# Kernel optimization log

Hardware: AMD Instinct MI355X
Metric: run time of the kernel (lower is better)

## Reference

```python
import jax, jax.numpy as jnp
import numpy as np

STRIDES = (4, 8, 16, 32, 64, 128)
MAPS = (128, 64, 32, 16, 8, 4)
VAR0, VAR1 = 0.1, 0.2
CLS_TH, NMS_TH, FINAL_TH = 0.05, 0.3, 0.5


def _decode_scale(ocls, oreg, stride):
    # ocls: [1,2,H,W], oreg: [1,4,H,W] -> dets [H*W, 5] = (x1,y1,x2,y2,score)
    prob = jax.nn.softmax(ocls, axis=1)[0, 1]          # [H,W] face probability
    H, W = prob.shape
    s = jnp.float32(stride)
    pcx = s / 2 + jnp.arange(W, dtype=jnp.float32)[None, :] * s   # prior center x
    pcy = s / 2 + jnp.arange(H, dtype=jnp.float32)[:, None] * s   # prior center y
    pwh = s * 4.0                                                 # prior w = h = 4*stride
    loc = oreg[0]                                                 # [4,H,W]
    cx = pcx + loc[0] * VAR0 * pwh
    cy = pcy + loc[1] * VAR0 * pwh
    w = pwh * jnp.exp(loc[2] * VAR1)
    h = pwh * jnp.exp(loc[3] * VAR1)
    x1 = cx - w / 2
    y1 = cy - h / 2
    x2 = x1 + w
    y2 = y1 + h
    return jnp.stack([x1.ravel(), y1.ravel(), x2.ravel(), y2.ravel(), prob.ravel()], axis=1)


def _nms_keep(dets, valid):
    # Greedy NMS (torch-style, +1 box convention), fixed trip count, returns keep mask.
    N = dets.shape[0]
    scores = jnp.where(valid, dets[:, 4], -jnp.inf)
    order = jnp.argsort(-scores)            # descending by score, invalid last
    b = dets[order]
    v = valid[order]
    x1, y1, x2, y2 = b[:, 0], b[:, 1], b[:, 2], b[:, 3]
    areas = (x2 - x1 + 1.0) * (y2 - y1 + 1.0)
    pos = jnp.arange(N)

    def body(i, carry):
        sup, keep = carry
        active = jnp.logical_and(jnp.logical_not(sup[i]), v[i])
        keep = keep.at[i].set(active)
        xx1 = jnp.maximum(x1[i], x1)
        yy1 = jnp.maximum(y1[i], y1)
        xx2 = jnp.minimum(x2[i], x2)
        yy2 = jnp.minimum(y2[i], y2)
        w = jnp.maximum(xx2 - xx1 + 1.0, 0.0)
        h = jnp.maximum(yy2 - yy1 + 1.0, 0.0)
        inter = w * h
        iou = inter / (areas[i] + areas - inter)
        sup = sup | (active & (iou > NMS_TH) & (pos > i))
        return sup, keep

    sup0 = jnp.logical_not(v)
    _, keep_sorted = jax.lax.fori_loop(0, N, body, (sup0, jnp.zeros(N, dtype=bool)))
    return jnp.zeros(N, dtype=bool).at[order].set(keep_sorted)


def _forward(ol1, ol2, ol3, ol4, ol5, ol6, ol7, ol8, ol9, ol10, ol11, ol12):
    olist = [ol1, ol2, ol3, ol4, ol5, ol6, ol7, ol8, ol9, ol10, ol11, ol12]
    dets = jnp.concatenate(
        [_decode_scale(olist[2 * i], olist[2 * i + 1], STRIDES[i]) for i in range(6)],
        axis=0)                              # [N,5]
    valid = dets[:, 4] > CLS_TH              # threshold stage (score > 0.05)
    # NMS selection is index logic -> constant w.r.t. differentiation
    keep = _nms_keep(jax.lax.stop_gradient(dets), valid)
    final = keep & (dets[:, 4] > FINAL_TH)   # post-NMS score > 0.5 filter
    # fixed-shape equivalent of gathering kept rows: zero out non-kept rows
    return dets * final[:, None].astype(dets.dtype)


def setup_inputs() -> dict:
    key = jax.random.key(0)
    inp = {}
    for i, hw in enumerate(MAPS):
        kc, kr, key = jax.random.split(key, 3)
        inp[f"ol{2 * i + 1}"] = jax.random.normal(kc, (1, 2, hw, hw), dtype=jnp.float32)
        inp[f"ol{2 * i + 2}"] = jax.random.normal(kr, (1, 4, hw, hw), dtype=jnp.float32)
    return inp


def reference(ol1, ol2, ol3, ol4, ol5, ol6, ol7, ol8, ol9, ol10, ol11, ol12):
    return _forward(ol1, ol2, ol3, ol4, ol5, ol6, ol7, ol8, ol9, ol10, ol11, ol12)
```

## Files before the change

kernel.cpp:

```cpp
#include <hip/hip_runtime.h>
#include <stdint.h>

#define N_TOTAL 21840
#define NA      21888
#define W_MAX   342
#define TOT_ENT 3753792u
#define NMS_TH  0.3f
#define FINAL_TH 0.5f
#define NSLICE  8
#define SLOTS   11
#define SCAN_T  768
#define NPUSH   11
#define GRP     4
#define NBAND   7
#define GMAX    86

struct Inputs { const float* cls[6]; const float* reg[6]; };

__device__ __forceinline__ void block_bar() {
  asm volatile("s_waitcnt lgkmcnt(0)\n\ts_barrier" ::: "memory");
}

__device__ __forceinline__ unsigned rowbase_u(unsigned r) {
  unsigned w = r >> 6, l = r & 63u;
  return 64u * (342u * w - (w * (w - 1u)) / 2u) + l * (342u - w);
}

__global__ void decode_kernel(Inputs in,
                              float* __restrict__ dx1, float* __restrict__ dy1,
                              float* __restrict__ dx2, float* __restrict__ dy2,
                              float* __restrict__ dsc,
                              unsigned long long* __restrict__ ckey,
                              unsigned int* __restrict__ Mc,
                              unsigned int* __restrict__ rank32,
                              unsigned int* __restrict__ cnt,
                              float* __restrict__ out) {
#pragma clang fp contract(off)
  int gid = blockIdx.x * blockDim.x + threadIdx.x;
  if (gid >= N_TOTAL) return;

  rank32[gid] = 0u;
  cnt[gid] = 0u;
  if (gid < NA - N_TOTAL) cnt[N_TOTAL + gid] = 0u;

  int sc, local;
  if      (gid < 16384) { sc = 0; local = gid;         }
  else if (gid < 20480) { sc = 1; local = gid - 16384; }
  else if (gid < 21504) { sc = 2; local = gid - 20480; }
  else if (gid < 21760) { sc = 3; local = gid - 21504; }
  else if (gid < 21824) { sc = 4; local = gid - 21760; }
  else                  { sc = 5; local = gid - 21824; }

  const int Wd     = 128 >> sc;
  const int stride = 4 << sc;
  const int HW     = Wd * Wd;
  const int x = local & (Wd - 1);
  const int y = local >> (7 - sc);

  const float* cls = in.cls[sc];
  const float* reg = in.reg[sc];

  float c0 = cls[local];
  float c1 = cls[HW + local];
  float m  = fmaxf(c0, c1);
  float e0 = expf(c0 - m);
  float e1 = expf(c1 - m);
  float prob = e1 / (e0 + e1);

  float l0 = reg[local];
  float l1 = reg[HW + local];
  float l2 = reg[2 * HW + local];
  float l3 = reg[3 * HW + local];

  float sF  = (float)stride;
  float pcx = 0.5f * sF + (float)x * sF;
  float pcy = 0.5f * sF + (float)y * sF;
  float pwh = sF * 4.0f;

  float cx = pcx + ((l0 * 0.1f) * pwh);
  float cy = pcy + ((l1 * 0.1f) * pwh);
  float w  = pwh * expf(l2 * 0.2f);
  float h  = pwh * expf(l3 * 0.2f);
  float x1 = cx - w * 0.5f;
  float y1 = cy - h * 0.5f;
  float x2 = x1 + w;
  float y2 = y1 + h;

  dx1[gid] = x1; dy1[gid] = y1; dx2[gid] = x2; dy2[gid] = y2; dsc[gid] = prob;

  out[gid * 5 + 0] = 0.0f;
  out[gid * 5 + 1] = 0.0f;
  out[gid * 5 + 2] = 0.0f;
  out[gid * 5 + 3] = 0.0f;
  out[gid * 5 + 4] = 0.0f;

  if (prob > FINAL_TH) {
    unsigned int pos = atomicAdd(Mc, 1u);
    ckey[pos] = ((unsigned long long)__float_as_uint(prob) << 32) |
                (unsigned int)(~(unsigned int)gid);
  }
}

__global__ void __launch_bounds__(256)
rank_kernel(const unsigned long long* __restrict__ ckey,
            const unsigned int* __restrict__ Mc,
            const float* __restrict__ dx1, const float* __restrict__ dy1,
            const float* __restrict__ dx2, const float* __restrict__ dy2,
            float* __restrict__ sx1, float* __restrict__ sy1,
            float* __restrict__ sx2, float* __restrict__ sy2,
            unsigned int* __restrict__ sorig,
            unsigned int* __restrict__ rank32) {
  __shared__ unsigned long long tile[256];
  const unsigned int M = *Mc;
  if (blockIdx.x * 256u >= M) return;
  const int t = (int)threadIdx.x;
  const int p = (int)blockIdx.x * 256 + t;
  unsigned long long mykey = (p < (int)M) ? ckey[p] : 0ull;
  const int S  = (int)((M + NSLICE - 1) / NSLICE);
  const int lo = (int)blockIdx.y * S;
  const int hi = min((int)M, lo + S);
  int partial = 0;
  const int nt = (hi > lo) ? ((hi - lo + 255) >> 8) : 0;
  for (int ti = 0; ti < nt; ++ti) {
    int j = lo + ti * 256 + t;
    tile[t] = (j < hi) ? ckey[j] : 0ull;
    __syncthreads();
#pragma unroll 8
    for (int q = 0; q < 256; ++q) partial += (tile[q] > mykey) ? 1 : 0;
    __syncthreads();
  }
  if (p < (int)M) {
    unsigned int pack = (unsigned int)partial | (1u << 24);
    unsigned int old  = atomicAdd(&rank32[p], pack);
    unsigned int newv = old + pack;
    if ((newv >> 24) == NSLICE) {
      int r = (int)(newv & 0xFFFFFF);
      unsigned int orig = ~(unsigned int)(mykey & 0xffffffffull);
      sx1[r] = dx1[orig];
      sy1[r] = dy1[orig];
      sx2[r] = dx2[orig];
      sy2[r] = dy2[orig];
      sorig[r] = orig;
    }
  }
}

__global__ void __launch_bounds__(1024)
pairs_kernel(const float* __restrict__ sx1, const float* __restrict__ sy1,
             const float* __restrict__ sx2, const float* __restrict__ sy2,
             const unsigned int* __restrict__ Mc,
             unsigned long long* __restrict__ diag,
             unsigned long long* __restrict__ bandT,
             unsigned int* __restrict__ cnt,
             unsigned short* __restrict__ rlJw,
             unsigned long long* __restrict__ rlBits) {
#pragma clang fp contract(off)
  const int M = (int)*Mc;
  const int W = (M + 63) >> 6;
  const int rw = (int)blockIdx.y;
  const int cwg = (int)blockIdx.x << 4;
  if (rw >= W || cwg >= W || cwg + 22 < rw) return;

  const int t = (int)threadIdx.x;
  const int g = t >> 6, l = t & 63;
  const int cw = cwg + g;

  __shared__ float cx1[1024], cy1[1024], cx2[1024], cy2[1024], car[1024];
  {
    int c = (cw << 6) + l;
    if (cw < W && c < M) {
      float a = sx1[c], b = sy1[c], d = sx2[c], e = sy2[c];
      cx1[t] = a; cy1[t] = b; cx2[t] = d; cy2[t] = e;
      car[t] = (d - a + 1.0f) * (e - b + 1.0f);
    }
  }
  __syncthreads();
  if (cw >= W) return;
  const int rwg = rw >> 2, cg = cw >> 2;
  const bool isDiag = (cw == rw);
  const bool isBand = (cw < rw) && (cg >= rwg - 1);
  const bool isCsr  = (cg >= rwg + 2);
  if (!isDiag && !isBand && !isCsr) return;

  const int r = (rw << 6) + l;
  unsigned long long bits = 0ull;
  if (r < M) {
    float ax1 = sx1[r], ay1 = sy1[r], ax2 = sx2[r], ay2 = sy2[r];
    float aarea = (ax2 - ax1 + 1.0f) * (ay2 - ay1 + 1.0f);
    const int cmax = min(64, M - (cw << 6));
    const int sb = g << 6;
    for (int cc = 0; cc < cmax; ++cc) {
      float xx1 = fmaxf(ax1, cx1[sb + cc]);
      float yy1 = fmaxf(ay1, cy1[sb + cc]);
      float xx2 = fminf(ax2, cx2[sb + cc]);
      float yy2 = fminf(ay2, cy2[sb + cc]);
      float ww = fmaxf(xx2 - xx1 + 1.0f, 0.0f);
      float hh = fmaxf(yy2 - yy1 + 1.0f, 0.0f);
      float inter = ww * hh;
      float iou = inter / (aarea + car[sb + cc] - inter);
      if (iou > NMS_TH) bits |= (1ull << cc);
    }
  }
  if (isDiag)      diag[r] = bits;
  else if (isBand) bandT[(size_t)(rw - cw - 1) * NA + r] = bits;
  else if (bits != 0ull) {
    unsigned k = atomicAdd(&cnt[r], 1u);
    unsigned b = rowbase_u((unsigned)r) + k;
    rlJw[b]   = (unsigned short)cw;
    rlBits[b] = bits;
  }
}

__global__ void __launch_bounds__(SCAN_T)
scan_kernel(const unsigned long long* __restrict__ diag,
            const unsigned long long* __restrict__ bandT,
            const unsigned int* __restrict__ cnt,
            const unsigned short* __restrict__ rlJw,
            const unsigned long long* __restrict__ rlBits,
            const unsigned int* __restrict__ sorig,
            const unsigned int* __restrict__ Mc,
            const float* __restrict__ dx1, const float* __restrict__ dy1,
            const float* __restrict__ dx2, const float* __restrict__ dy2,
            const float* __restrict__ dsc,
            float* __restrict__ out) {
  __shared__ unsigned long long sup[W_MAX];
  __shared__ unsigned long long kmls[W_MAX];
  __shared__ unsigned gdone[GMAX];
  __shared__ volatile unsigned sflag;
  const int t = (int)threadIdx.x;
  const int g = t >> 6, l = t & 63;
  const int M = (int)*Mc;
  const int W = (M + 63) >> 6;
  const int NS = (W + 3) >> 2;

  for (int i = t; i < W_MAX; i += SCAN_T) { sup[i] = 0ull; kmls[i] = 0ull; }
  for (int i = t; i < GMAX; i += SCAN_T) gdone[i] = 0u;
  if (t == 0) sflag = 0u;
  block_bar();

  if (g == 0) {
    __builtin_amdgcn_s_setprio(1);
    const unsigned long long lowm = (1ull << l) - 1ull;
    unsigned long long dc[4], dn[4];
    unsigned long long bc[4][NBAND], bn[4][NBAND];
    unsigned long long kp[4] = {0ull, 0ull, 0ull, 0ull};
#pragma unroll
    for (int i = 0; i < 4; ++i) {
      int v = i, vc = (v < W) ? v : 0;
      dc[i] = diag[(vc << 6) + l];
#pragma unroll
      for (int d = 1; d <= NBAND; ++d)
        if (d <= i + 4) bc[i][d - 1] = bandT[(size_t)(d - 1) * NA + (vc << 6) + l];
    }
#pragma unroll
    for (int i = 0; i < 4; ++i) {
      int v = 4 + i, vc = (v < W) ? v : 0;
      dn[i] = diag[(vc << 6) + l];
#pragma unroll
      for (int d = 1; d <= NBAND; ++d)
        if (d <= i + 4) bn[i][d - 1] = bandT[(size_t)(d - 1) * NA + (vc << 6) + l];
    }
    for (int s = 0; s < NS; ++s) {
      const int v0 = s << 2;
      unsigned long long accp[4];
#pragma unroll
      for (int i = 0; i < 4; ++i) {
        unsigned long long a = 0ull;
#pragma unroll
        for (int d = 1; d <= NBAND; ++d)
          if (d <= i + 4 && d > i) a |= (bc[i][d - 1] & kp[i - d + 4]);
        accp[i] = a;
      }
      if (s >= 2) {
        while (*(volatile unsigned*)&gdone[s - 2] < (unsigned)NPUSH) {}
        asm volatile("" ::: "memory");
      }
      unsigned long long sv[4];
#pragma unroll
      for (int i = 0; i < 4; ++i)
        sv[i] = (v0 + i < W) ? sup[v0 + i] : 0ull;
      unsigned long long kc[4];
#pragma unroll
      for (int i = 0; i < 4; ++i) {
        const int v = v0 + i;
        unsigned long long kept = 0ull;
        if (v < W) {
          unsigned long long acc = accp[i];
#pragma unroll
          for (int d = 1; d <= 3; ++d)
            if (d <= i) acc |= (bc[i][d - 1] & kc[i - d]);
          unsigned long long incoming = __ballot(acc != 0ull);
          const int n = min(64, M - (v << 6));
          unsigned long long wm = (n >= 64) ? ~0ull : ((1ull << n) - 1ull);
          unsigned long long pend = (~(sv[i] | incoming)) & wm;
          const unsigned long long dv = dc[i] & lowm;
          unsigned long long dead = ~pend, und = pend;
          while (und) {
            unsigned long long bS = __ballot((dv & kept) != 0ull) & und;
            unsigned long long bK = __ballot((dv & ~dead) == 0ull) & und;
            kept |= bK; dead |= bS; und &= ~(bK | bS);
          }
          if (l == i) kmls[v] = kept;
        }
        kc[i] = kept;
      }
      asm volatile("s_waitcnt lgkmcnt(0)" ::: "memory");
      if (l == 0) sflag = (unsigned)(s + 1);
#pragma unroll
      for (int i = 0; i < 4; ++i) kp[i] = kc[i];
#pragma unroll
      for (int i = 0; i < 4; ++i) {
        dc[i] = dn[i];
#pragma unroll
        for (int d = 0; d < NBAND; ++d)
          if (d <= i + 3) bc[i][d] = bn[i][d];
      }
      const int vn = v0 + 8;
#pragma unroll
      for (int i = 0; i < 4; ++i) {
        int v = vn + i, vc = (v < W) ? v : 0;
        dn[i] = diag[(vc << 6) + l];
#pragma unroll
        for (int d = 1; d <= NBAND; ++d)
          if (d <= i + 4) bn[i][d - 1] = bandT[(size_t)(d - 1) * NA + (vc << 6) + l];
      }
    }
    __builtin_amdgcn_s_setprio(0);
  } else {
    const int p = (g - 1) * 64 + l;
    const int jrow = p / SLOTS;
    const int sub  = p % SLOTS;
    unsigned cc[4], nc[4];
    unsigned long long cb[4], nb[4];
    unsigned cj[4], nj[4];
#pragma unroll
    for (int i = 0; i < 4; ++i) {
      int w = i, wc = (w < W) ? w : 0;
      cc[i] = cnt[(wc << 6) + jrow];
      unsigned idx = rowbase_u((unsigned)((wc << 6) + jrow)) + sub;
      if (idx >= TOT_ENT) idx = 0;
      cb[i] = rlBits[idx]; cj[i] = (unsigned)rlJw[idx];
    }
#pragma unroll
    for (int i = 0; i < 4; ++i) {
      int w = 4 + i, wc = (w < W) ? w : 0;
      nc[i] = cnt[(wc << 6) + jrow];
      unsigned idx = rowbase_u((unsigned)((wc << 6) + jrow)) + sub;
      if (idx >= TOT_ENT) idx = 0;
      nb[i] = rlBits[idx]; nj[i] = (unsigned)rlJw[idx];
    }
    for (int s = 0; s < NS; ++s) {
      while (sflag < (unsigned)(s + 1)) __builtin_amdgcn_s_sleep(1);
      asm volatile("" ::: "memory");
      const int v0 = s << 2;
#pragma unroll
      for (int i = 0; i < 4; ++i) {
        const int w = v0 + i;
        const unsigned long long km = (w < W) ? kmls[w] : 0ull;
        if ((km >> jrow) & 1ull) {
          if (sub < (int)cc[i]) atomicOr(&sup[cj[i]], cb[i]);
          if (cc[i] > (unsigned)SLOTS) {
            unsigned rb_ = rowbase_u((unsigned)((w << 6) + jrow));
            for (int k = sub + SLOTS; k < (int)cc[i]; k += SLOTS) {
              unsigned ii2 = rb_ + k;
              atomicOr(&sup[rlJw[ii2]], rlBits[ii2]);
            }
          }
        }
      }
      asm volatile("s_waitcnt lgkmcnt(0)" ::: "memory");
      if (l == 0) atomicAdd(&gdone[s], 1u);
#pragma unroll
      for (int i = 0; i < 4; ++i) { cc[i] = nc[i]; cb[i] = nb[i]; cj[i] = nj[i]; }
      const int w0 = v0 + 8;
#pragma unroll
      for (int i = 0; i < 4; ++i) {
        int w = w0 + i, wc = (w < W) ? w : 0;
        nc[i] = cnt[(wc << 6) + jrow];
        unsigned idx = rowbase_u((unsigned)((wc << 6) + jrow)) + sub;
        if (idx >= TOT_ENT) idx = 0;
        nb[i] = rlBits[idx]; nj[i] = (unsigned)rlJw[idx];
      }
    }
  }
  block_bar();

  for (int i = t; i < (W << 6); i += SCAN_T) {
    if ((kmls[i >> 6] >> (i & 63)) & 1ull) {
      unsigned int orig = sorig[i];
      out[(size_t)orig * 5 + 0] = dx1[orig];
      out[(size_t)orig * 5 + 1] = dy1[orig];
      out[(size_t)orig * 5 + 2] = dx2[orig];
      out[(size_t)orig * 5 + 3] = dy2[orig];
      out[(size_t)orig * 5 + 4] = dsc[orig];
    }
  }
}

__global__ void __launch_bounds__(1024)
nms_kernel(const float* __restrict__ sx1, const float* __restrict__ sy1,
           const float* __restrict__ sx2, const float* __restrict__ sy2,
           const unsigned int* __restrict__ sorig,
           const unsigned int* __restrict__ Mc,
           unsigned int* __restrict__ keepflag) {
#pragma clang fp contract(off)
  __shared__ unsigned long long sup[W_MAX];
  __shared__ unsigned long long inrow[64];
  __shared__ float wx1[64], wy1[64], wx2[64], wy2[64], warea[64];
  __shared__ unsigned long long keptmask_sh;

  const int t = (int)threadIdx.x;
  const int M = (int)*Mc;
  const int W = (M + 63) >> 6;

  for (int i = t; i < W_MAX; i += 1024) sup[i] = 0ull;
  __syncthreads();

  for (int w = 0; w < W; ++w) {
    const int base = w << 6;
    const int n = min(64, M - base);
    if (t < 64) {
      if (t < n) {
        float a = sx1[base + t], b = sy1[base + t];
        float c = sx2[base + t], d = sy2[base + t];
        wx1[t] = a; wy1[t] = b; wx2[t] = c; wy2[t] = d;
        warea[t] = (c - a + 1.0f) * (d - b + 1.0f);
      }
    } else if (t < 128) {
      inrow[t - 64] = 0ull;
    }
    __syncthreads();
    {
      int r = t & 63, seg = t >> 6;
      unsigned long long bits = 0ull;
      if (r < n) {
        float ax1 = wx1[r], ay1 = wy1[r], ax2 = wx2[r], ay2 = wy2[r];
        float aarea = warea[r];
        for (int c = seg * 4; c < seg * 4 + 4; ++c) {
          if (c > r && c < n) {
            float xx1 = fmaxf(ax1, wx1[c]);
            float yy1 = fmaxf(ay1, wy1[c]);
            float xx2 = fminf(ax2, wx2[c]);
            float yy2 = fminf(ay2, wy2[c]);
            float ww = fmaxf(xx2 - xx1 + 1.0f, 0.0f);
            float hh = fmaxf(yy2 - yy1 + 1.0f, 0.0f);
            float inter = ww * hh;
            float iou = inter / (aarea + warea[c] - inter);
            if (iou > NMS_TH) bits |= (1ull << c);
          }
        }
      }
      if (bits) atomicOr(&inrow[r], bits);
    }
    __syncthreads();
    if (t < 64) {
      unsigned long long wordmask = (n >= 64) ? ~0ull : ((1ull << n) - 1ull);
      unsigned long long pending = (~sup[w]) & wordmask;
      unsigned long long kept = 0ull;
      while (pending) {
        int i = __builtin_ctzll(pending);
        kept |= (1ull << i);
        pending &= ~(inrow[i] | (1ull << i));
      }
      if (t == 0) keptmask_sh = kept;
      if (t < n && ((kept >> t) & 1ull)) keepflag[sorig[base + t]] = 1u;
    }
    __syncthreads();
    unsigned long long km = keptmask_sh;
    if (km) {
      int wid = t >> 6, lane = t & 63;
      for (int jw = w + 1 + wid; (jw << 6) < M; jw += 16) {
        int j = (jw << 6) + lane;
        bool supj = false;
        if (j < M) {
          float jx1 = sx1[j], jy1 = sy1[j], jx2 = sx2[j], jy2 = sy2[j];
          float jarea = (jx2 - jx1 + 1.0f) * (jy2 - jy1 + 1.0f);
          unsigned long long mm = km;
          while (mm) {
            int r = __builtin_ctzll(mm);
            mm &= mm - 1ull;
            float xx1 = fmaxf(wx1[r], jx1);
            float yy1 = fmaxf(wy1[r], jy1);
            float xx2 = fminf(wx2[r], jx2);
            float yy2 = fminf(wy2[r], jy2);
            float ww = fmaxf(xx2 - xx1 + 1.0f, 0.0f);
            float hh = fmaxf(yy2 - yy1 + 1.0f, 0.0f);
            float inter = ww * hh;
            float iou = inter / (warea[r] + jarea - inter);
            if (iou > NMS_TH) { supj = true; break; }
          }
        }
        unsigned long long bal = __ballot(supj);
        if (lane == 0 && bal) atomicOr(&sup[jw], bal);
      }
    }
    __syncthreads();
  }
}

__global__ void output_kernel(const float* __restrict__ dx1, const float* __restrict__ dy1,
                              const float* __restrict__ dx2, const float* __restrict__ dy2,
                              const float* __restrict__ dsc,
                              const unsigned int* __restrict__ keepflag,
                              float* __restrict__ out) {
#pragma clang fp contract(off)
  int gid = blockIdx.x * blockDim.x + threadIdx.x;
  if (gid >= N_TOTAL) return;
  float f = keepflag[gid] ? 1.0f : 0.0f;
  out[gid * 5 + 0] = dx1[gid] * f;
  out[gid * 5 + 1] = dy1[gid] * f;
  out[gid * 5 + 2] = dx2[gid] * f;
  out[gid * 5 + 3] = dy2[gid] * f;
  out[gid * 5 + 4] = dsc[gid] * f;
}

extern "C" void kernel_launch(void* const* d_in, const int* in_sizes, int n_in,
                              void* d_out, int out_size, void* d_ws, size_t ws_size,
                              hipStream_t stream) {
  (void)in_sizes; (void)n_in; (void)out_size;

  Inputs in;
  for (int i = 0; i < 6; ++i) {
    in.cls[i] = (const float*)d_in[2 * i];
    in.reg[i] = (const float*)d_in[2 * i + 1];
  }

  char* ws = (char*)d_ws;
  size_t o = 0;
  float* dx1 = (float*)(ws + o); o += (size_t)NA * 4;
  float* dy1 = (float*)(ws + o); o += (size_t)NA * 4;
  float* dx2 = (float*)(ws + o); o += (size_t)NA * 4;
  float* dy2 = (float*)(ws + o); o += (size_t)NA * 4;
  float* dsc = (float*)(ws + o); o += (size_t)NA * 4;
  unsigned long long* ckey = (unsigned long long*)(ws + o); o += (size_t)NA * 8;
  float* sx1 = (float*)(ws + o); o += (size_t)NA * 4;
  float* sy1 = (float*)(ws + o); o += (size_t)NA * 4;
  float* sx2 = (float*)(ws + o); o += (size_t)NA * 4;
  float* sy2 = (float*)(ws + o); o += (size_t)NA * 4;
  unsigned int* sorig = (unsigned int*)(ws + o); o += (size_t)NA * 4;
  unsigned int* keepflag = (unsigned int*)(ws + o); o += (size_t)NA * 4;
  unsigned int* rank32 = (unsigned int*)(ws + o); o += (size_t)NA * 4;
  unsigned int* cnt = (unsigned int*)(ws + o); o += (size_t)NA * 4;
  unsigned int* Mc = (unsigned int*)(ws + o); o += 64;
  o = (o + 511) & ~(size_t)511;
  unsigned long long* diag = (unsigned long long*)(ws + o); o += (size_t)NA * 8;
  unsigned long long* bandT = (unsigned long long*)(ws + o); o += (size_t)NBAND * NA * 8;
  unsigned long long* rlBits = (unsigned long long*)(ws + o); o += (size_t)TOT_ENT * 8;
  unsigned short* rlJw = (unsigned short*)(ws + o); o += (size_t)TOT_ENT * 2;
  size_t need = o;
  const bool fast = (need <= ws_size);

  const int nb = (N_TOTAL + 255) / 256;

  if (fast) {
    (void)hipMemsetAsync((void*)Mc, 0, 64, stream);
    decode_kernel<<<nb, 256, 0, stream>>>(in, dx1, dy1, dx2, dy2, dsc, ckey, Mc,
                                          rank32, cnt, (float*)d_out);
    rank_kernel<<<dim3(nb, NSLICE), 256, 0, stream>>>(ckey, Mc, dx1, dy1, dx2, dy2,
                                                      sx1, sy1, sx2, sy2, sorig,
                                                      rank32);
    pairs_kernel<<<dim3(22, W_MAX), 1024, 0, stream>>>(sx1, sy1, sx2, sy2, Mc,
                                                       diag, bandT, cnt, rlJw, rlBits);
    scan_kernel<<<1, SCAN_T, 0, stream>>>(diag, bandT, cnt, rlJw, rlBits, sorig, Mc,
                                          dx1, dy1, dx2, dy2, dsc, (float*)d_out);
  } else {
    (void)hipMemsetAsync((void*)keepflag, 0, (size_t)NA * 12 + 64, stream);
    decode_kernel<<<nb, 256, 0, stream>>>(in, dx1, dy1, dx2, dy2, dsc, ckey, Mc,
                                          rank32, cnt, (float*)d_out);
    rank_kernel<<<dim3(nb, NSLICE), 256, 0, stream>>>(ckey, Mc, dx1, dy1, dx2, dy2,
                                                      sx1, sy1, sx2, sy2, sorig,
                                                      rank32);
    nms_kernel<<<1, 1024, 0, stream>>>(sx1, sy1, sx2, sy2, sorig, Mc, keepflag);
    output_kernel<<<nb, 256, 0, stream>>>(dx1, dy1, dx2, dy2, dsc, keepflag,
                                          (float*)d_out);
  }
}
```

Before: 260.8 us.

## Pack far-pair suppression lists per row-word with wave-aggregated atomics

The per-row suppression lists for off-band column words become one packed list per 64-row word. Entries are allocated with one wave-wide atomic per row-word using a ballot and popcount, and each entry stores the row lane alongside the column word. The scan kernel's helper waves now stream the compacted list with a strided, software-prefetched loop and filter entries by the kept-row mask, instead of fixed per-row slots plus overflow loops. This removes per-thread atomics and the load imbalance of rows with many entries. In exchange, every entry in a word is read even when few of its rows are kept, and the up-front prefetch of upcoming words is dropped.

```diff
diff --git a/kernel.cpp b/kernel.cpp
--- a/kernel.cpp
+++ b/kernel.cpp
@@ -8,7 +8,6 @@
 #define NMS_TH  0.3f
 #define FINAL_TH 0.5f
 #define NSLICE  8
-#define SLOTS   11
 #define SCAN_T  768
 #define NPUSH   11
 #define GRP     4
@@ -21,9 +20,8 @@
   asm volatile("s_waitcnt lgkmcnt(0)\n\ts_barrier" ::: "memory");
 }
 
-__device__ __forceinline__ unsigned rowbase_u(unsigned r) {
-  unsigned w = r >> 6, l = r & 63u;
-  return 64u * (342u * w - (w * (w - 1u)) / 2u) + l * (342u - w);
+__device__ __forceinline__ unsigned wbase_u(unsigned w) {
+  return 64u * (342u * w - (w * (w - 1u)) / 2u);
 }
 
 __global__ void decode_kernel(Inputs in,
@@ -33,15 +31,15 @@
                               unsigned long long* __restrict__ ckey,
                               unsigned int* __restrict__ Mc,
                               unsigned int* __restrict__ rank32,
-                              unsigned int* __restrict__ cnt,
+                              unsigned int* __restrict__ wcnt,
                               float* __restrict__ out) {
 #pragma clang fp contract(off)
   int gid = blockIdx.x * blockDim.x + threadIdx.x;
   if (gid >= N_TOTAL) return;
 
   rank32[gid] = 0u;
-  cnt[gid] = 0u;
-  if (gid < NA - N_TOTAL) cnt[N_TOTAL + gid] = 0u;
+  wcnt[gid] = 0u;
+  if (gid < NA - N_TOTAL) wcnt[N_TOTAL + gid] = 0u;
 
   int sc, local;
   if      (gid < 16384) { sc = 0; local = gid;         }
@@ -151,8 +149,8 @@
              const unsigned int* __restrict__ Mc,
              unsigned long long* __restrict__ diag,
              unsigned long long* __restrict__ bandT,
-             unsigned int* __restrict__ cnt,
-             unsigned short* __restrict__ rlJw,
+             unsigned int* __restrict__ wcnt,
+             unsigned short* __restrict__ rlMeta,
              unsigned long long* __restrict__ rlBits) {
 #pragma clang fp contract(off)
   const int M = (int)*Mc;
@@ -203,19 +201,28 @@
   }
   if (isDiag)      diag[r] = bits;
   else if (isBand) bandT[(size_t)(rw - cw - 1) * NA + r] = bits;
-  else if (bits != 0ull) {
-    unsigned k = atomicAdd(&cnt[r], 1u);
-    unsigned b = rowbase_u((unsigned)r) + k;
-    rlJw[b]   = (unsigned short)cw;
-    rlBits[b] = bits;
+  else {
+    unsigned long long ball = __ballot(bits != 0ull);
+    if (ball) {
+      unsigned n_ = (unsigned)__popcll(ball);
+      unsigned base = 0u;
+      if (l == 0) base = atomicAdd(&wcnt[rw], n_);
+      base = (unsigned)__shfl((int)base, 0);
+      if (bits != 0ull) {
+        unsigned rank = (unsigned)__popcll(ball & ((1ull << l) - 1ull));
+        unsigned slot = wbase_u((unsigned)rw) + base + rank;
+        rlMeta[slot] = (unsigned short)(((unsigned)l << 9) | (unsigned)cw);
+        rlBits[slot] = bits;
+      }
+    }
   }
 }
 
 __global__ void __launch_bounds__(SCAN_T)
 scan_kernel(const unsigned long long* __restrict__ diag,
             const unsigned long long* __restrict__ bandT,
-            const unsigned int* __restrict__ cnt,
-            const unsigned short* __restrict__ rlJw,
+            const unsigned int* __restrict__ wcnt,
+            const unsigned short* __restrict__ rlMeta,
             const unsigned long long* __restrict__ rlBits,
             const unsigned int* __restrict__ sorig,
             const unsigned int* __restrict__ Mc,
@@ -225,6 +232,7 @@
             float* __restrict__ out) {
   __shared__ unsigned long long sup[W_MAX];
   __shared__ unsigned long long kmls[W_MAX];
+  __shared__ unsigned lds_wcnt[W_MAX];
   __shared__ unsigned gdone[GMAX];
   __shared__ volatile unsigned sflag;
   const int t = (int)threadIdx.x;
@@ -233,7 +241,9 @@
   const int W = (M + 63) >> 6;
   const int NS = (W + 3) >> 2;
 
-  for (int i = t; i < W_MAX; i += SCAN_T) { sup[i] = 0ull; kmls[i] = 0ull; }
+  for (int i = t; i < W_MAX; i += SCAN_T) {
+    sup[i] = 0ull; kmls[i] = 0ull; lds_wcnt[i] = wcnt[i];
+  }
   for (int i = t; i < GMAX; i += SCAN_T) gdone[i] = 0u;
   if (t == 0) sflag = 0u;
   block_bar();
@@ -328,59 +338,38 @@
     __builtin_amdgcn_s_setprio(0);
   } else {
     const int p = (g - 1) * 64 + l;
-    const int jrow = p / SLOTS;
-    const int sub  = p % SLOTS;
-    unsigned cc[4], nc[4];
-    unsigned long long cb[4], nb[4];
-    unsigned cj[4], nj[4];
-#pragma unroll
-    for (int i = 0; i < 4; ++i) {
-      int w = i, wc = (w < W) ? w : 0;
-      cc[i] = cnt[(wc << 6) + jrow];
-      unsigned idx = rowbase_u((unsigned)((wc << 6) + jrow)) + sub;
-      if (idx >= TOT_ENT) idx = 0;
-      cb[i] = rlBits[idx]; cj[i] = (unsigned)rlJw[idx];
-    }
-#pragma unroll
-    for (int i = 0; i < 4; ++i) {
-      int w = 4 + i, wc = (w < W) ? w : 0;
-      nc[i] = cnt[(wc << 6) + jrow];
-      unsigned idx = rowbase_u((unsigned)((wc << 6) + jrow)) + sub;
-      if (idx >= TOT_ENT) idx = 0;
-      nb[i] = rlBits[idx]; nj[i] = (unsigned)rlJw[idx];
-    }
     for (int s = 0; s < NS; ++s) {
       while (sflag < (unsigned)(s + 1)) __builtin_amdgcn_s_sleep(1);
       asm volatile("" ::: "memory");
       const int v0 = s << 2;
 #pragma unroll
       for (int i = 0; i < 4; ++i) {
-        const int w = v0 + i;
-        const unsigned long long km = (w < W) ? kmls[w] : 0ull;
-        if ((km >> jrow) & 1ull) {
-          if (sub < (int)cc[i]) atomicOr(&sup[cj[i]], cb[i]);
-          if (cc[i] > (unsigned)SLOTS) {
-            unsigned rb_ = rowbase_u((unsigned)((w << 6) + jrow));
-            for (int k = sub + SLOTS; k < (int)cc[i]; k += SLOTS) {
-              unsigned ii2 = rb_ + k;
-              atomicOr(&sup[rlJw[ii2]], rlBits[ii2]);
-            }
+        const int v = v0 + i;
+        if (v >= W) continue;
+        const unsigned tw = lds_wcnt[v];
+        if (tw == 0u) continue;
+        const unsigned long long km = kmls[v];
+        if (km == 0ull) continue;
+        const unsigned base = wbase_u((unsigned)v);
+        unsigned idx = base + (unsigned)p;
+        const unsigned end = base + tw;
+        if (idx < end) {
+          unsigned mm0 = (unsigned)rlMeta[idx];
+          unsigned long long bb0 = rlBits[idx];
+          for (;;) {
+            unsigned nidx = idx + (unsigned)(NPUSH * 64);
+            bool has = (nidx < end);
+            unsigned mm1 = has ? (unsigned)rlMeta[nidx] : 0u;
+            unsigned long long bb1 = has ? rlBits[nidx] : 0ull;
+            if ((km >> (mm0 >> 9)) & 1ull)
+              atomicOr(&sup[mm0 & 511u], bb0);
+            if (!has) break;
+            idx = nidx; mm0 = mm1; bb0 = bb1;
           }
         }
       }
       asm volatile("s_waitcnt lgkmcnt(0)" ::: "memory");
       if (l == 0) atomicAdd(&gdone[s], 1u);
-#pragma unroll
-      for (int i = 0; i < 4; ++i) { cc[i] = nc[i]; cb[i] = nb[i]; cj[i] = nj[i]; }
-      const int w0 = v0 + 8;
-#pragma unroll
-      for (int i = 0; i < 4; ++i) {
-        int w = w0 + i, wc = (w < W) ? w : 0;
-        nc[i] = cnt[(wc << 6) + jrow];
-        unsigned idx = rowbase_u((unsigned)((wc << 6) + jrow)) + sub;
-        if (idx >= TOT_ENT) idx = 0;
-        nb[i] = rlBits[idx]; nj[i] = (unsigned)rlJw[idx];
-      }
     }
   }
   block_bar();
@@ -540,13 +529,13 @@
   unsigned int* sorig = (unsigned int*)(ws + o); o += (size_t)NA * 4;
   unsigned int* keepflag = (unsigned int*)(ws + o); o += (size_t)NA * 4;
   unsigned int* rank32 = (unsigned int*)(ws + o); o += (size_t)NA * 4;
-  unsigned int* cnt = (unsigned int*)(ws + o); o += (size_t)NA * 4;
+  unsigned int* wcnt = (unsigned int*)(ws + o); o += (size_t)NA * 4;
   unsigned int* Mc = (unsigned int*)(ws + o); o += 64;
   o = (o + 511) & ~(size_t)511;
   unsigned long long* diag = (unsigned long long*)(ws + o); o += (size_t)NA * 8;
   unsigned long long* bandT = (unsigned long long*)(ws + o); o += (size_t)NBAND * NA * 8;
   unsigned long long* rlBits = (unsigned long long*)(ws + o); o += (size_t)TOT_ENT * 8;
-  unsigned short* rlJw = (unsigned short*)(ws + o); o += (size_t)TOT_ENT * 2;
+  unsigned short* rlMeta = (unsigned short*)(ws + o); o += (size_t)TOT_ENT * 2;
   size_t need = o;
   const bool fast = (need <= ws_size);
 
@@ -555,18 +544,18 @@
   if (fast) {
     (void)hipMemsetAsync((void*)Mc, 0, 64, stream);
     decode_kernel<<<nb, 256, 0, stream>>>(in, dx1, dy1, dx2, dy2, dsc, ckey, Mc,
-                                          rank32, cnt, (float*)d_out);
+                                          rank32, wcnt, (float*)d_out);
     rank_kernel<<<dim3(nb, NSLICE), 256, 0, stream>>>(ckey, Mc, dx1, dy1, dx2, dy2,
                                                       sx1, sy1, sx2, sy2, sorig,
                                                       rank32);
     pairs_kernel<<<dim3(22, W_MAX), 1024, 0, stream>>>(sx1, sy1, sx2, sy2, Mc,
-                                                       diag, bandT, cnt, rlJw, rlBits);
-    scan_kernel<<<1, SCAN_T, 0, stream>>>(diag, bandT, cnt, rlJw, rlBits, sorig, Mc,
+                                                       diag, bandT, wcnt, rlMeta, rlBits);
+    scan_kernel<<<1, SCAN_T, 0, stream>>>(diag, bandT, wcnt, rlMeta, rlBits, sorig, Mc,
                                           dx1, dy1, dx2, dy2, dsc, (float*)d_out);
   } else {
     (void)hipMemsetAsync((void*)keepflag, 0, (size_t)NA * 12 + 64, stream);
     decode_kernel<<<nb, 256, 0, stream>>>(in, dx1, dy1, dx2, dy2, dsc, ckey, Mc,
-                                          rank32, cnt, (float*)d_out);
+                                          rank32, wcnt, (float*)d_out);
     rank_kernel<<<dim3(nb, NSLICE), 256, 0, stream>>>(ckey, Mc, dx1, dy1, dx2, dy2,
                                                       sx1, sy1, sx2, sy2, sorig,
                                                       rank32);
```

Result: slower. 307.8 us (+18.0%).
